# Performance work log

Hardware: AMD Instinct MI355X
Metric: run time of the kernel (lower is better)

Reference implementation:

```python
import jax, jax.numpy as jnp
import numpy as np

B, L, D, H, DK, DV = 2, 2048, 1024, 16, 64, 64
NEG_INF = -100000000.0


def setup_inputs() -> dict:
    key = jax.random.key(0)
    ks = jax.random.split(key, 10)
    s = 0.02
    inp = {
        "q": jax.random.normal(ks[0], (B, L, D), jnp.float32),
        "k": jax.random.normal(ks[1], (B, L, D), jnp.float32),
        "v": jax.random.normal(ks[2], (B, L, D), jnp.float32),
        "Wq": jax.random.normal(ks[3], (D, H * DK), jnp.float32) * s,
        "bq": jnp.zeros((H * DK,), jnp.float32),
        "Wk": jax.random.normal(ks[4], (D, H * DK), jnp.float32) * s,
        "bk": jnp.zeros((H * DK,), jnp.float32),
        "Wv": jax.random.normal(ks[5], (D, H * DV), jnp.float32) * s,
        "bv": jnp.zeros((H * DV,), jnp.float32),
        "W0": jax.random.normal(ks[6], (H * DV, D), jnp.float32) * s,
        "b0": jnp.zeros((D,), jnp.float32),
        "key_padding_mask": jax.random.uniform(ks[7], (B, L)) < 0.1,
        # 3D causal mask (B, Lq, Lk); True = masked
        "attn_mask": jnp.broadcast_to(jnp.triu(jnp.ones((L, L), bool), k=1), (B, L, L)),
    }
    return inp


def reference(q, k, v, Wq, bq, Wk, bk, Wv, bv, W0, b0, key_padding_mask, attn_mask):
    b, lq, _ = q.shape
    lk = k.shape[1]
    dk = Wq.shape[1] // H
    dv = Wv.shape[1] // H
    qh = (q @ Wq + bq).reshape(b, lq, H, dk)  # (B,Lq,H,dk)
    kh = (k @ Wk + bk).reshape(b, lk, H, dk)
    vh = (v @ Wv + bv).reshape(b, lk, H, dv)
    # scaled scores (B,H,Lq,Lk)
    attn = jnp.einsum("bqhd,bkhd->bhqk", qh, kh) / jnp.sqrt(jnp.float32(dk))
    # attn_mask (B,Lq,Lk): masked_fill semantics
    attn = jnp.where(attn_mask[:, None, :, :], NEG_INF, attn)
    # key_padding_mask (B,Lq): masks full query rows (broadcast over keys)
    attn = jnp.where(key_padding_mask[:, None, :, None], NEG_INF, attn)
    attn = jax.nn.softmax(attn, axis=-1)
    out = jnp.einsum("bhqk,bkhd->bqhd", attn, vh).reshape(b, lq, H * dv)
    out = out @ W0 + b0  # (B,Lq,D)
    return out, attn
```

## Files before the change

### kernel.cpp

```cpp
#include <hip/hip_runtime.h>

#define B_ 2
#define L_ 2048
#define D_ 1024
#define H_ 16
#define DKV 64
#define NEG_INF -1e8f

typedef float f32x4 __attribute__((ext_vector_type(4)));
typedef __bf16 bf16x8 __attribute__((ext_vector_type(8)));
typedef unsigned int u32x4 __attribute__((ext_vector_type(4)));
typedef unsigned int u32x2 __attribute__((ext_vector_type(2)));
typedef unsigned short u16x4 __attribute__((ext_vector_type(4)));

__device__ __forceinline__ unsigned short f2bfbits(float f) {
  unsigned int u = __builtin_bit_cast(unsigned int, f);
  unsigned int r = (u + 0x7FFFu + ((u >> 16) & 1u)) >> 16;
  return (unsigned short)r;
}
__device__ __forceinline__ __bf16 f2bf(float f) {
  return __builtin_bit_cast(__bf16, f2bfbits(f));
}
__device__ __forceinline__ float bf2f(unsigned short b) {
  unsigned int u = ((unsigned int)b) << 16;
  return __builtin_bit_cast(float, u);
}

__global__ __launch_bounds__(256) void norm_kpm_k(const void* __restrict__ raw,
                                                  unsigned char* __restrict__ kpmn) {
  __shared__ int flag;
  const int tid = threadIdx.x;
  if (tid == 0) flag = 0;
  __syncthreads();
  const unsigned* w = (const unsigned*)raw;
  unsigned bad = 0;
  for (int i = tid; i < 1024; i += 256) bad |= (w[i] > 1u) ? 1u : 0u;
  if (bad) flag = 1;
  __syncthreads();
  const bool u8 = (flag != 0);
  const unsigned char* u = (const unsigned char*)raw;
  for (int i = tid; i < B_ * L_; i += 256)
    kpmn[i] = u8 ? (u[i] != 0) : (w[i] != 0);
}

__global__ __launch_bounds__(256) void convert_x_k(
    const float* __restrict__ xq, const float* __restrict__ xk, const float* __restrict__ xv,
    unsigned short* __restrict__ oq, unsigned short* __restrict__ ok, unsigned short* __restrict__ ov)
{
  const int proj = blockIdx.y;
  const float* X = proj == 0 ? xq : (proj == 1 ? xk : xv);
  unsigned short* O = proj == 0 ? oq : (proj == 1 ? ok : ov);
  const long i8 = ((long)blockIdx.x * 256 + threadIdx.x) * 8;
  f32x4 a = *(const f32x4*)(X + i8);
  f32x4 b = *(const f32x4*)(X + i8 + 4);
  u32x4 p;
  p[0] = (unsigned)f2bfbits(a[0]) | ((unsigned)f2bfbits(a[1]) << 16);
  p[1] = (unsigned)f2bfbits(a[2]) | ((unsigned)f2bfbits(a[3]) << 16);
  p[2] = (unsigned)f2bfbits(b[0]) | ((unsigned)f2bfbits(b[1]) << 16);
  p[3] = (unsigned)f2bfbits(b[2]) | ((unsigned)f2bfbits(b[3]) << 16);
  *(u32x4*)(O + i8) = p;
}

__global__ __launch_bounds__(256) void convert_wt_k(
    const float* __restrict__ Wq, const float* __restrict__ Wk,
    const float* __restrict__ Wv, const float* __restrict__ W0,
    unsigned short* __restrict__ Wtq, unsigned short* __restrict__ Wtk,
    unsigned short* __restrict__ Wtv, unsigned short* __restrict__ W0t)
{
  __shared__ float Tl[64][65];
  const int m = blockIdx.z;
  const float* W = m == 0 ? Wq : (m == 1 ? Wk : (m == 2 ? Wv : W0));
  unsigned short* Wt = m == 0 ? Wtq : (m == 1 ? Wtk : (m == 2 ? Wtv : W0t));
  const int k0 = blockIdx.x * 64, n0 = blockIdx.y * 64;
  const int tid = threadIdx.x;
  #pragma unroll
  for (int it = 0; it < 4; ++it) {
    int idx = it * 256 + tid;
    int r = idx >> 4, c4 = (idx & 15) << 2;
    f32x4 x = *(const f32x4*)(W + (long)(k0 + r) * 1024 + n0 + c4);
    Tl[r][c4] = x[0]; Tl[r][c4 + 1] = x[1]; Tl[r][c4 + 2] = x[2]; Tl[r][c4 + 3] = x[3];
  }
  __syncthreads();
  #pragma unroll
  for (int it = 0; it < 2; ++it) {
    int idx = it * 256 + tid;
    int n = idx >> 3, c8 = (idx & 7) << 3;
    u32x4 p;
    #pragma unroll
    for (int j = 0; j < 4; ++j)
      p[j] = (unsigned)f2bfbits(Tl[c8 + 2 * j][n]) | ((unsigned)f2bfbits(Tl[c8 + 2 * j + 1][n]) << 16);
    *(u32x4*)(Wt + (long)(n0 + n) * 1024 + k0 + c8) = p;
  }
}

__global__ __launch_bounds__(256) void colsum_part_k(const unsigned short* __restrict__ vh,
                                                     float* __restrict__ part) {
  __shared__ float red[4][64];
  const int bid = blockIdx.x, tid = threadIdx.x;
  const int z = bid >> 3, seg = bid & 7;
  const int col = tid & 63, rgrp = tid >> 6;
  const long zoff = (long)z * L_ * DKV;
  float s = 0.f;
  #pragma unroll 4
  for (int i = 0; i < 64; ++i) {
    int r = seg * 256 + rgrp + 4 * i;
    s += bf2f(vh[zoff + (long)r * DKV + col]);
  }
  red[rgrp][col] = s;
  __syncthreads();
  if (tid < 64)
    part[(long)bid * 64 + tid] = red[0][tid] + red[1][tid] + red[2][tid] + red[3][tid];
}

__global__ __launch_bounds__(64) void colsum_final_k(const float* __restrict__ part,
                                                     float* __restrict__ colsumV) {
  const int z = blockIdx.x, col = threadIdx.x;
  float s = 0.f;
  #pragma unroll
  for (int seg = 0; seg < 8; ++seg) s += part[((long)z * 8 + seg) * 64 + col];
  colsumV[z * DKV + col] = s;
}

__global__ __launch_bounds__(256) void qkv_gemm_k(
    const unsigned short* __restrict__ xqb, const unsigned short* __restrict__ xkb,
    const unsigned short* __restrict__ xvb,
    const unsigned short* __restrict__ Wtq, const unsigned short* __restrict__ Wtk,
    const unsigned short* __restrict__ Wtv,
    const float* __restrict__ bq, const float* __restrict__ bk, const float* __restrict__ bv,
    unsigned short* __restrict__ oq, unsigned short* __restrict__ ok, unsigned short* __restrict__ ov)
{
  __shared__ __align__(16) unsigned short Al[128][72];
  __shared__ __align__(16) unsigned short Bl[128][72];
  const int proj = blockIdx.y;
  const unsigned short* X  = proj == 0 ? xqb : (proj == 1 ? xkb : xvb);
  const unsigned short* Wt = proj == 0 ? Wtq : (proj == 1 ? Wtk : Wtv);
  const float* bias = proj == 0 ? bq : (proj == 1 ? bk : bv);
  unsigned short* O = proj == 0 ? oq : (proj == 1 ? ok : ov);
  const int mt = blockIdx.x, zp = blockIdx.z;
  const int bb = zp >> 3, hp = zp & 7;
  const int tid = threadIdx.x, lane = tid & 63, w = tid >> 6, g = lane >> 4, l16 = lane & 15;
  const int wm = w >> 1, wn = w & 1;
  const long arow0 = (long)bb * L_ + mt * 128;
  const long brow0 = (long)hp * 128;

  const f32x4 zero4 = {0.f, 0.f, 0.f, 0.f};
  f32x4 acc[4][4];
  #pragma unroll
  for (int i = 0; i < 4; ++i)
    #pragma unroll
    for (int j = 0; j < 4; ++j) acc[i][j] = zero4;

  for (int kt = 0; kt < D_; kt += 64) {
    #pragma unroll
    for (int it = 0; it < 4; ++it) {
      int idx = it * 256 + tid;
      int r = idx >> 3, c8 = (idx & 7) << 3;
      *(u32x4*)&Al[r][c8] = *(const u32x4*)(X + (arow0 + r) * D_ + kt + c8);
      *(u32x4*)&Bl[r][c8] = *(const u32x4*)(Wt + (brow0 + r) * D_ + kt + c8);
    }
    __syncthreads();
    #pragma unroll
    for (int ks = 0; ks < 2; ++ks) {
      bf16x8 a[4], bv8[4];
      #pragma unroll
      for (int fm = 0; fm < 4; ++fm)
        a[fm] = *(const bf16x8*)&Al[wm * 64 + fm * 16 + l16][ks * 32 + g * 8];
      #pragma unroll
      for (int fn = 0; fn < 4; ++fn)
        bv8[fn] = *(const bf16x8*)&Bl[wn * 64 + fn * 16 + l16][ks * 32 + g * 8];
      #pragma unroll
      for (int fm = 0; fm < 4; ++fm)
        #pragma unroll
        for (int fn = 0; fn < 4; ++fn)
          acc[fm][fn] = __builtin_amdgcn_mfma_f32_16x16x32_bf16(a[fm], bv8[fn], acc[fm][fn], 0, 0, 0);
    }
    __syncthreads();
  }
  #pragma unroll
  for (int fm = 0; fm < 4; ++fm)
    #pragma unroll
    for (int fn = 0; fn < 4; ++fn)
      #pragma unroll
      for (int r = 0; r < 4; ++r) {
        int row = mt * 128 + wm * 64 + fm * 16 + g * 4 + r;
        int col = wn * 64 + fn * 16 + l16;
        float val = acc[fm][fn][r] + bias[hp * 128 + col];
        int zh = bb * H_ + hp * 2 + (col >> 6);
        O[(long)zh * L_ * 64 + (long)row * 64 + (col & 63)] = f2bfbits(val);
      }
}

__global__ __launch_bounds__(256) void oproj_gemm_k(
    const unsigned short* __restrict__ Ab, const unsigned short* __restrict__ W0t,
    const float* __restrict__ b0, float* __restrict__ out)
{
  __shared__ __align__(16) unsigned short Al[64][72];
  __shared__ __align__(16) unsigned short Bl[128][72];
  const int mt = blockIdx.x, nt = blockIdx.y;
  const int tid = threadIdx.x, lane = tid & 63, w = tid >> 6, g = lane >> 4, l16 = lane & 15;
  const int wm = w >> 1, wn = w & 1;

  const f32x4 zero4 = {0.f, 0.f, 0.f, 0.f};
  f32x4 acc[2][4];
  #pragma unroll
  for (int i = 0; i < 2; ++i)
    #pragma unroll
    for (int j = 0; j < 4; ++j) acc[i][j] = zero4;

  for (int kt = 0; kt < D_; kt += 64) {
    #pragma unroll
    for (int it = 0; it < 2; ++it) {
      int idx = it * 256 + tid;
      int r = idx >> 3, c8 = (idx & 7) << 3;
      *(u32x4*)&Al[r][c8] = *(const u32x4*)(Ab + (long)(mt * 64 + r) * D_ + kt + c8);
    }
    #pragma unroll
    for (int it = 0; it < 4; ++it) {
      int idx = it * 256 + tid;
      int r = idx >> 3, c8 = (idx & 7) << 3;
      *(u32x4*)&Bl[r][c8] = *(const u32x4*)(W0t + (long)(nt * 128 + r) * D_ + kt + c8);
    }
    __syncthreads();
    #pragma unroll
    for (int ks = 0; ks < 2; ++ks) {
      bf16x8 a[2], bv8[4];
      #pragma unroll
      for (int fm = 0; fm < 2; ++fm)
        a[fm] = *(const bf16x8*)&Al[wm * 32 + fm * 16 + l16][ks * 32 + g * 8];
      #pragma unroll
      for (int fn = 0; fn < 4; ++fn)
        bv8[fn] = *(const bf16x8*)&Bl[wn * 64 + fn * 16 + l16][ks * 32 + g * 8];
      #pragma unroll
      for (int fm = 0; fm < 2; ++fm)
        #pragma unroll
        for (int fn = 0; fn < 4; ++fn)
          acc[fm][fn] = __builtin_amdgcn_mfma_f32_16x16x32_bf16(a[fm], bv8[fn], acc[fm][fn], 0, 0, 0);
    }
    __syncthreads();
  }
  #pragma unroll
  for (int fm = 0; fm < 2; ++fm)
    #pragma unroll
    for (int fn = 0; fn < 4; ++fn)
      #pragma unroll
      for (int r = 0; r < 4; ++r) {
        int row = mt * 64 + wm * 32 + fm * 16 + g * 4 + r;
        int col = nt * 128 + wn * 64 + fn * 16 + l16;
        out[(long)row * D_ + col] = acc[fm][fn][r] + b0[col];
      }
}

__global__ __launch_bounds__(256) void attn_pv_k(
    const unsigned short* __restrict__ qh, const unsigned short* __restrict__ kh,
    const unsigned short* __restrict__ vh, const unsigned char* __restrict__ kpm,
    const float* __restrict__ colsumV, float* __restrict__ attn,
    unsigned short* __restrict__ oh)
{
  __shared__ __align__(16) char smem[64 * 68 * 4];
  auto Ql = (unsigned short (*)[72])smem;
  auto Pl = (float (*)[68])smem;
  __shared__ __align__(16) unsigned short Kl[64][72];
  __shared__ __align__(16) unsigned short Vl[64][72];
  __shared__ unsigned char padl[64];

  const int tid = threadIdx.x, lane = tid & 63, w = tid >> 6, g = lane >> 4, l16 = lane & 15;
  const int bid = blockIdx.x;
  const int z = bid & 31;
  const int sx = bid >> 5;
  const int q0 = sx * 64;
  const int b = z >> 4, h = z & 15;
  const long zoff = (long)z * L_ * DKV;
  const int rowbase = q0 + w * 16 + g * 4;

  #pragma unroll
  for (int it = 0; it < 2; ++it) {
    int f = it * 256 + tid;
    int r = f >> 3, c8 = (f & 7) << 3;
    *(u32x4*)&Ql[r][c8] = *(const u32x4*)(qh + zoff + (long)(q0 + r) * 64 + c8);
  }
  if (tid < 64) padl[tid] = kpm[b * L_ + q0 + tid];
  __syncthreads();
  bf16x8 a[2];
  #pragma unroll
  for (int ks = 0; ks < 2; ++ks)
    a[ks] = *(const bf16x8*)&Ql[w * 16 + l16][ks * 32 + g * 8];
  bool pad[4];
  #pragma unroll
  for (int r = 0; r < 4; ++r) pad[r] = padl[w * 16 + g * 4 + r] != 0;
  __syncthreads();

  float psum[4] = {0.f, 0.f, 0.f, 0.f};
  const f32x4 zero4 = {0.f, 0.f, 0.f, 0.f};
  f32x4 o[4];
  #pragma unroll
  for (int fn = 0; fn < 4; ++fn) o[fn] = zero4;

  for (int kt = 0; kt <= sx; ++kt) {
    #pragma unroll
    for (int it = 0; it < 2; ++it) {
      int f = it * 256 + tid;
      int r = f >> 3, c8 = (f & 7) << 3;
      *(u32x4*)&Kl[r][c8] = *(const u32x4*)(kh + zoff + (long)(kt * 64 + r) * 64 + c8);
    }
    #pragma unroll
    for (int it = 0; it < 4; ++it) {
      int f = it * 256 + tid;
      int kk = f >> 4, n4 = (f & 15) << 2;
      u16x4 u = *(const u16x4*)(vh + zoff + (long)(kt * 64 + kk) * 64 + n4);
      int sw = kk ^ (((n4 >> 2) & 7) << 3);
      Vl[n4 + 0][sw] = u[0]; Vl[n4 + 1][sw] = u[1];
      Vl[n4 + 2][sw] = u[2]; Vl[n4 + 3][sw] = u[3];
    }
    __syncthreads();
    f32x4 s[4];
    #pragma unroll
    for (int fn = 0; fn < 4; ++fn) {
      bf16x8 bv0 = *(const bf16x8*)&Kl[fn * 16 + l16][g * 8];
      bf16x8 bv1 = *(const bf16x8*)&Kl[fn * 16 + l16][32 + g * 8];
      f32x4 t = zero4;
      t = __builtin_amdgcn_mfma_f32_16x16x32_bf16(a[0], bv0, t, 0, 0, 0);
      t = __builtin_amdgcn_mfma_f32_16x16x32_bf16(a[1], bv1, t, 0, 0, 0);
      s[fn] = t;
    }
    #pragma unroll
    for (int fn = 0; fn < 4; ++fn)
      #pragma unroll
      for (int r = 0; r < 4; ++r) {
        int kk = kt * 64 + fn * 16 + l16;
        float sv = s[fn][r] * 0.125f;
        if (kk > rowbase + r) sv = NEG_INF;
        float p = __expf(sv - 12.0f);
        psum[r] += p;
        Pl[w * 16 + g * 4 + r][fn * 16 + l16] = p;
      }
    bf16x8 pa[2];
    #pragma unroll
    for (int ks = 0; ks < 2; ++ks) {
      f32x4 lo = *(const f32x4*)&Pl[w * 16 + l16][ks * 32 + g * 8];
      f32x4 hi = *(const f32x4*)&Pl[w * 16 + l16][ks * 32 + g * 8 + 4];
      bf16x8 t;
      #pragma unroll
      for (int i = 0; i < 4; ++i) { t[i] = f2bf(lo[i]); t[i + 4] = f2bf(hi[i]); }
      pa[ks] = t;
    }
    #pragma unroll
    for (int fn = 0; fn < 4; ++fn) {
      int dv = fn * 16 + l16;
      int swz = ((dv >> 2) & 7) << 3;
      bf16x8 vb0 = *(const bf16x8*)&Vl[dv][(0 * 32 + g * 8) ^ swz];
      bf16x8 vb1 = *(const bf16x8*)&Vl[dv][(1 * 32 + g * 8) ^ swz];
      o[fn] = __builtin_amdgcn_mfma_f32_16x16x32_bf16(pa[0], vb0, o[fn], 0, 0, 0);
      o[fn] = __builtin_amdgcn_mfma_f32_16x16x32_bf16(pa[1], vb1, o[fn], 0, 0, 0);
    }
    __syncthreads();
  }

  float linv[4];
  #pragma unroll
  for (int r = 0; r < 4; ++r) {
    float s = psum[r];
    #pragma unroll
    for (int d = 1; d < 16; d <<= 1) s += __shfl_xor(s, d);
    linv[r] = 1.f / s;
  }
  const float invL = 1.0f / (float)L_;

  float* arow = attn + ((long)z * L_ + q0 + w * 16) * L_;
  for (int kt = 0; kt <= sx; ++kt) {
    #pragma unroll
    for (int it = 0; it < 2; ++it) {
      int f = it * 256 + tid;
      int r = f >> 3, c8 = (f & 7) << 3;
      *(u32x4*)&Kl[r][c8] = *(const u32x4*)(kh + zoff + (long)(kt * 64 + r) * 64 + c8);
    }
    __syncthreads();
    f32x4 s[4];
    #pragma unroll
    for (int fn = 0; fn < 4; ++fn) {
      bf16x8 bv0 = *(const bf16x8*)&Kl[fn * 16 + l16][g * 8];
      bf16x8 bv1 = *(const bf16x8*)&Kl[fn * 16 + l16][32 + g * 8];
      f32x4 t = zero4;
      t = __builtin_amdgcn_mfma_f32_16x16x32_bf16(a[0], bv0, t, 0, 0, 0);
      t = __builtin_amdgcn_mfma_f32_16x16x32_bf16(a[1], bv1, t, 0, 0, 0);
      s[fn] = t;
    }
    #pragma unroll
    for (int fn = 0; fn < 4; ++fn)
      #pragma unroll
      for (int r = 0; r < 4; ++r) {
        int kk = kt * 64 + fn * 16 + l16;
        float sv = s[fn][r] * 0.125f;
        if (kk > rowbase + r) sv = NEG_INF;
        float p = pad[r] ? invL : __expf(sv - 12.0f) * linv[r];
        __builtin_nontemporal_store(p, &arow[(long)(g * 4 + r) * L_ + kt * 64 + fn * 16 + l16]);
      }
    __syncthreads();
  }
  for (int kt = sx + 1; kt < L_ / 64; ++kt) {
    #pragma unroll
    for (int it = 0; it < 4; ++it) {
      int f = it * 256 + tid;
      int r = f >> 4, c4 = (f & 15) << 2;
      float vvv = padl[r] ? invL : 0.f;
      f32x4 ov = {vvv, vvv, vvv, vvv};
      __builtin_nontemporal_store(ov, (f32x4*)&attn[((long)z * L_ + q0 + r) * L_ + kt * 64 + c4]);
    }
  }

  #pragma unroll
  for (int fn = 0; fn < 4; ++fn)
    #pragma unroll
    for (int r = 0; r < 4; ++r) {
      int qq = rowbase + r;
      int dv = fn * 16 + l16;
      float val = pad[r] ? invL * colsumV[z * DKV + dv] : o[fn][r] * linv[r];
      oh[((long)b * L_ + qq) * (H_ * DKV) + h * DKV + dv] = f2bfbits(val);
    }
}

extern "C" void kernel_launch(void* const* d_in, const int* in_sizes, int n_in,
                              void* d_out, int out_size, void* d_ws, size_t ws_size,
                              hipStream_t stream) {
  (void)in_sizes; (void)n_in; (void)out_size; (void)ws_size;
  const float* q  = (const float*)d_in[0];
  const float* k  = (const float*)d_in[1];
  const float* v  = (const float*)d_in[2];
  const float* Wq = (const float*)d_in[3];
  const float* bq = (const float*)d_in[4];
  const float* Wk = (const float*)d_in[5];
  const float* bk = (const float*)d_in[6];
  const float* Wv = (const float*)d_in[7];
  const float* bv = (const float*)d_in[8];
  const float* W0 = (const float*)d_in[9];
  const float* b0 = (const float*)d_in[10];
  const void*  kpm_raw = d_in[11];

  float* out  = (float*)d_out;
  float* attn = out + (long)B_ * L_ * D_;

  const long XE = (long)B_ * L_ * D_;
  const long HEAD_ELEMS = (long)B_ * H_ * L_ * DKV;
  unsigned short* qh  = (unsigned short*)d_ws;
  unsigned short* kh  = qh + HEAD_ELEMS;
  unsigned short* vh  = kh + HEAD_ELEMS;
  unsigned short* xqb = vh + HEAD_ELEMS;
  unsigned short* xkb = xqb + XE;
  unsigned short* xvb = xkb + XE;
  unsigned short* oh  = xqb;
  unsigned short* Wtq = xvb + XE;
  unsigned short* Wtk = Wtq + (long)D_ * D_;
  unsigned short* Wtv = Wtk + (long)D_ * D_;
  unsigned short* W0t = Wtv + (long)D_ * D_;
  float* colsumV = (float*)(W0t + (long)D_ * D_);
  float* part    = colsumV + 32 * 64;
  unsigned char* kpmn = (unsigned char*)(part + 256 * 64);

  dim3 blk(256);

  norm_kpm_k<<<1, blk, 0, stream>>>(kpm_raw, kpmn);
  convert_x_k<<<dim3(XE / (256 * 8), 3), blk, 0, stream>>>(q, k, v, xqb, xkb, xvb);
  convert_wt_k<<<dim3(16, 16, 4), blk, 0, stream>>>(Wq, Wk, Wv, W0, Wtq, Wtk, Wtv, W0t);

  qkv_gemm_k<<<dim3(L_ / 128, 3, B_ * (H_ / 2)), blk, 0, stream>>>(
      xqb, xkb, xvb, Wtq, Wtk, Wtv, bq, bk, bv, qh, kh, vh);

  colsum_part_k<<<dim3(256), blk, 0, stream>>>(vh, part);
  colsum_final_k<<<dim3(32), dim3(64), 0, stream>>>(part, colsumV);

  attn_pv_k<<<dim3(1024), blk, 0, stream>>>(
      qh, kh, vh, kpmn, colsumV, attn, oh);

  oproj_gemm_k<<<dim3(B_ * L_ / 64, D_ / 128), blk, 0, stream>>>(
      oh, W0t, b0, out);
}
```

Baseline: 259.8 us.

## Merge prep kernels and register-prefetch K/V tiles in attention kernel

Three preprocessing kernels (mask normalisation, activation conversion, weight transpose) become one launch dispatched by block index, saving launch overhead. The attention kernel now prefetches the next K/V tile into registers while the current tile is computed. Its second pass handles two K tiles per barrier by reusing the V shared buffer, which halves the syncs. A launch-bounds occupancy hint of 4 is added, which may limit registers and risk spills.

```diff
diff --git a/kernel.cpp b/kernel.cpp
--- a/kernel.cpp
+++ b/kernel.cpp
@@ -26,70 +26,68 @@
   return __builtin_bit_cast(float, u);
 }
 
-__global__ __launch_bounds__(256) void norm_kpm_k(const void* __restrict__ raw,
-                                                  unsigned char* __restrict__ kpmn) {
-  __shared__ int flag;
-  const int tid = threadIdx.x;
-  if (tid == 0) flag = 0;
-  __syncthreads();
-  const unsigned* w = (const unsigned*)raw;
-  unsigned bad = 0;
-  for (int i = tid; i < 1024; i += 256) bad |= (w[i] > 1u) ? 1u : 0u;
-  if (bad) flag = 1;
-  __syncthreads();
-  const bool u8 = (flag != 0);
-  const unsigned char* u = (const unsigned char*)raw;
-  for (int i = tid; i < B_ * L_; i += 256)
-    kpmn[i] = u8 ? (u[i] != 0) : (w[i] != 0);
-}
-
-__global__ __launch_bounds__(256) void convert_x_k(
+__global__ __launch_bounds__(256) void prep_k(
     const float* __restrict__ xq, const float* __restrict__ xk, const float* __restrict__ xv,
-    unsigned short* __restrict__ oq, unsigned short* __restrict__ ok, unsigned short* __restrict__ ov)
-{
-  const int proj = blockIdx.y;
-  const float* X = proj == 0 ? xq : (proj == 1 ? xk : xv);
-  unsigned short* O = proj == 0 ? oq : (proj == 1 ? ok : ov);
-  const long i8 = ((long)blockIdx.x * 256 + threadIdx.x) * 8;
-  f32x4 a = *(const f32x4*)(X + i8);
-  f32x4 b = *(const f32x4*)(X + i8 + 4);
-  u32x4 p;
-  p[0] = (unsigned)f2bfbits(a[0]) | ((unsigned)f2bfbits(a[1]) << 16);
-  p[1] = (unsigned)f2bfbits(a[2]) | ((unsigned)f2bfbits(a[3]) << 16);
-  p[2] = (unsigned)f2bfbits(b[0]) | ((unsigned)f2bfbits(b[1]) << 16);
-  p[3] = (unsigned)f2bfbits(b[2]) | ((unsigned)f2bfbits(b[3]) << 16);
-  *(u32x4*)(O + i8) = p;
-}
-
-__global__ __launch_bounds__(256) void convert_wt_k(
     const float* __restrict__ Wq, const float* __restrict__ Wk,
     const float* __restrict__ Wv, const float* __restrict__ W0,
+    const void* __restrict__ kpm_raw,
+    unsigned short* __restrict__ oq, unsigned short* __restrict__ ok, unsigned short* __restrict__ ov,
     unsigned short* __restrict__ Wtq, unsigned short* __restrict__ Wtk,
-    unsigned short* __restrict__ Wtv, unsigned short* __restrict__ W0t)
+    unsigned short* __restrict__ Wtv, unsigned short* __restrict__ W0t,
+    unsigned char* __restrict__ kpmn)
 {
   __shared__ float Tl[64][65];
-  const int m = blockIdx.z;
-  const float* W = m == 0 ? Wq : (m == 1 ? Wk : (m == 2 ? Wv : W0));
-  unsigned short* Wt = m == 0 ? Wtq : (m == 1 ? Wtk : (m == 2 ? Wtv : W0t));
-  const int k0 = blockIdx.x * 64, n0 = blockIdx.y * 64;
-  const int tid = threadIdx.x;
-  #pragma unroll
-  for (int it = 0; it < 4; ++it) {
-    int idx = it * 256 + tid;
-    int r = idx >> 4, c4 = (idx & 15) << 2;
-    f32x4 x = *(const f32x4*)(W + (long)(k0 + r) * 1024 + n0 + c4);
-    Tl[r][c4] = x[0]; Tl[r][c4 + 1] = x[1]; Tl[r][c4 + 2] = x[2]; Tl[r][c4 + 3] = x[3];
-  }
-  __syncthreads();
-  #pragma unroll
-  for (int it = 0; it < 2; ++it) {
-    int idx = it * 256 + tid;
-    int n = idx >> 3, c8 = (idx & 7) << 3;
+  const int bid = blockIdx.x, tid = threadIdx.x;
+  if (bid < 6144) {
+    const int proj = bid >> 11;
+    const float* X = proj == 0 ? xq : (proj == 1 ? xk : xv);
+    unsigned short* O = proj == 0 ? oq : (proj == 1 ? ok : ov);
+    const long i8 = ((long)(bid & 2047) * 256 + tid) * 8;
+    f32x4 a = *(const f32x4*)(X + i8);
+    f32x4 b = *(const f32x4*)(X + i8 + 4);
     u32x4 p;
-    #pragma unroll
-    for (int j = 0; j < 4; ++j)
-      p[j] = (unsigned)f2bfbits(Tl[c8 + 2 * j][n]) | ((unsigned)f2bfbits(Tl[c8 + 2 * j + 1][n]) << 16);
-    *(u32x4*)(Wt + (long)(n0 + n) * 1024 + k0 + c8) = p;
+    p[0] = (unsigned)f2bfbits(a[0]) | ((unsigned)f2bfbits(a[1]) << 16);
+    p[1] = (unsigned)f2bfbits(a[2]) | ((unsigned)f2bfbits(a[3]) << 16);
+    p[2] = (unsigned)f2bfbits(b[0]) | ((unsigned)f2bfbits(b[1]) << 16);
+    p[3] = (unsigned)f2bfbits(b[2]) | ((unsigned)f2bfbits(b[3]) << 16);
+    *(u32x4*)(O + i8) = p;
+  } else if (bid < 7168) {
+    const int wid = bid - 6144;
+    const int m = wid >> 8, t = wid & 255;
+    const float* W = m == 0 ? Wq : (m == 1 ? Wk : (m == 2 ? Wv : W0));
+    unsigned short* Wt = m == 0 ? Wtq : (m == 1 ? Wtk : (m == 2 ? Wtv : W0t));
+    const int k0 = ((t >> 4) & 15) * 64, n0 = (t & 15) * 64;
+    #pragma unroll
+    for (int it = 0; it < 4; ++it) {
+      int idx = it * 256 + tid;
+      int r = idx >> 4, c4 = (idx & 15) << 2;
+      f32x4 x = *(const f32x4*)(W + (long)(k0 + r) * 1024 + n0 + c4);
+      Tl[r][c4] = x[0]; Tl[r][c4 + 1] = x[1]; Tl[r][c4 + 2] = x[2]; Tl[r][c4 + 3] = x[3];
+    }
+    __syncthreads();
+    #pragma unroll
+    for (int it = 0; it < 2; ++it) {
+      int idx = it * 256 + tid;
+      int n = idx >> 3, c8 = (idx & 7) << 3;
+      u32x4 p;
+      #pragma unroll
+      for (int j = 0; j < 4; ++j)
+        p[j] = (unsigned)f2bfbits(Tl[c8 + 2 * j][n]) | ((unsigned)f2bfbits(Tl[c8 + 2 * j + 1][n]) << 16);
+      *(u32x4*)(Wt + (long)(n0 + n) * 1024 + k0 + c8) = p;
+    }
+  } else {
+    __shared__ int flag;
+    if (tid == 0) flag = 0;
+    __syncthreads();
+    const unsigned* w = (const unsigned*)kpm_raw;
+    unsigned bad = 0;
+    for (int i = tid; i < 1024; i += 256) bad |= (w[i] > 1u) ? 1u : 0u;
+    if (bad) flag = 1;
+    __syncthreads();
+    const bool u8 = (flag != 0);
+    const unsigned char* u = (const unsigned char*)kpm_raw;
+    for (int i = tid; i < B_ * L_; i += 256)
+      kpmn[i] = u8 ? (u[i] != 0) : (w[i] != 0);
   }
 }
 
@@ -250,7 +248,7 @@
       }
 }
 
-__global__ __launch_bounds__(256) void attn_pv_k(
+__global__ __launch_bounds__(256, 4) void attn_pv_k(
     const unsigned short* __restrict__ qh, const unsigned short* __restrict__ kh,
     const unsigned short* __restrict__ vh, const unsigned char* __restrict__ kpm,
     const float* __restrict__ colsumV, float* __restrict__ attn,
@@ -272,6 +270,9 @@
   const long zoff = (long)z * L_ * DKV;
   const int rowbase = q0 + w * 16 + g * 4;
 
+  const int kr = tid >> 3, kc8 = (tid & 7) << 3;
+  const int vk = tid >> 4, vn4 = (tid & 15) << 2;
+
   #pragma unroll
   for (int it = 0; it < 2; ++it) {
     int f = it * 256 + tid;
@@ -295,23 +296,36 @@
   #pragma unroll
   for (int fn = 0; fn < 4; ++fn) o[fn] = zero4;
 
+  u32x4 Kreg[2];
+  u16x4 Vreg[4];
+  #pragma unroll
+  for (int it = 0; it < 2; ++it)
+    Kreg[it] = *(const u32x4*)(kh + zoff + (long)(kr + it * 32) * 64 + kc8);
+  #pragma unroll
+  for (int it = 0; it < 4; ++it)
+    Vreg[it] = *(const u16x4*)(vh + zoff + (long)(vk + it * 16) * 64 + vn4);
+
   for (int kt = 0; kt <= sx; ++kt) {
     #pragma unroll
-    for (int it = 0; it < 2; ++it) {
-      int f = it * 256 + tid;
-      int r = f >> 3, c8 = (f & 7) << 3;
-      *(u32x4*)&Kl[r][c8] = *(const u32x4*)(kh + zoff + (long)(kt * 64 + r) * 64 + c8);
-    }
+    for (int it = 0; it < 2; ++it)
+      *(u32x4*)&Kl[kr + it * 32][kc8] = Kreg[it];
     #pragma unroll
     for (int it = 0; it < 4; ++it) {
-      int f = it * 256 + tid;
-      int kk = f >> 4, n4 = (f & 15) << 2;
-      u16x4 u = *(const u16x4*)(vh + zoff + (long)(kt * 64 + kk) * 64 + n4);
-      int sw = kk ^ (((n4 >> 2) & 7) << 3);
-      Vl[n4 + 0][sw] = u[0]; Vl[n4 + 1][sw] = u[1];
-      Vl[n4 + 2][sw] = u[2]; Vl[n4 + 3][sw] = u[3];
-    }
-    __syncthreads();
+      int kk = vk + it * 16;
+      int sw = kk ^ (((vn4 >> 2) & 7) << 3);
+      Vl[vn4 + 0][sw] = Vreg[it][0]; Vl[vn4 + 1][sw] = Vreg[it][1];
+      Vl[vn4 + 2][sw] = Vreg[it][2]; Vl[vn4 + 3][sw] = Vreg[it][3];
+    }
+    __syncthreads();
+    if (kt < sx) {
+      const long noff = zoff + (long)((kt + 1) * 64) * 64;
+      #pragma unroll
+      for (int it = 0; it < 2; ++it)
+        Kreg[it] = *(const u32x4*)(kh + noff + (long)(kr + it * 32) * 64 + kc8);
+      #pragma unroll
+      for (int it = 0; it < 4; ++it)
+        Vreg[it] = *(const u16x4*)(vh + noff + (long)(vk + it * 16) * 64 + vn4);
+    }
     f32x4 s[4];
     #pragma unroll
     for (int fn = 0; fn < 4; ++fn) {
@@ -366,15 +380,35 @@
   const float invL = 1.0f / (float)L_;
 
   float* arow = attn + ((long)z * L_ + q0 + w * 16) * L_;
-  for (int kt = 0; kt <= sx; ++kt) {
-    #pragma unroll
-    for (int it = 0; it < 2; ++it) {
-      int f = it * 256 + tid;
-      int r = f >> 3, c8 = (f & 7) << 3;
-      *(u32x4*)&Kl[r][c8] = *(const u32x4*)(kh + zoff + (long)(kt * 64 + r) * 64 + c8);
-    }
-    __syncthreads();
-    f32x4 s[4];
+  u32x4 K2reg[2];
+  #pragma unroll
+  for (int it = 0; it < 2; ++it)
+    Kreg[it] = *(const u32x4*)(kh + zoff + (long)(kr + it * 32) * 64 + kc8);
+  if (1 <= sx)
+    #pragma unroll
+    for (int it = 0; it < 2; ++it)
+      K2reg[it] = *(const u32x4*)(kh + zoff + (long)(64 + kr + it * 32) * 64 + kc8);
+
+  for (int kt = 0; kt <= sx; kt += 2) {
+    const bool has2 = (kt + 1 <= sx);
+    #pragma unroll
+    for (int it = 0; it < 2; ++it)
+      *(u32x4*)&Kl[kr + it * 32][kc8] = Kreg[it];
+    if (has2)
+      #pragma unroll
+      for (int it = 0; it < 2; ++it)
+        *(u32x4*)&Vl[kr + it * 32][kc8] = K2reg[it];
+    __syncthreads();
+    if (kt + 2 <= sx) {
+      const long noff = zoff + (long)((kt + 2) * 64) * 64;
+      #pragma unroll
+      for (int it = 0; it < 2; ++it)
+        Kreg[it] = *(const u32x4*)(kh + noff + (long)(kr + it * 32) * 64 + kc8);
+      if (kt + 3 <= sx)
+        #pragma unroll
+        for (int it = 0; it < 2; ++it)
+          K2reg[it] = *(const u32x4*)(kh + noff + (long)(64 + kr + it * 32) * 64 + kc8);
+    }
     #pragma unroll
     for (int fn = 0; fn < 4; ++fn) {
       bf16x8 bv0 = *(const bf16x8*)&Kl[fn * 16 + l16][g * 8];
@@ -382,18 +416,33 @@
       f32x4 t = zero4;
       t = __builtin_amdgcn_mfma_f32_16x16x32_bf16(a[0], bv0, t, 0, 0, 0);
       t = __builtin_amdgcn_mfma_f32_16x16x32_bf16(a[1], bv1, t, 0, 0, 0);
-      s[fn] = t;
-    }
-    #pragma unroll
-    for (int fn = 0; fn < 4; ++fn)
       #pragma unroll
       for (int r = 0; r < 4; ++r) {
         int kk = kt * 64 + fn * 16 + l16;
-        float sv = s[fn][r] * 0.125f;
+        float sv = t[r] * 0.125f;
         if (kk > rowbase + r) sv = NEG_INF;
         float p = pad[r] ? invL : __expf(sv - 12.0f) * linv[r];
-        __builtin_nontemporal_store(p, &arow[(long)(g * 4 + r) * L_ + kt * 64 + fn * 16 + l16]);
+        __builtin_nontemporal_store(p, &arow[(long)(g * 4 + r) * L_ + kk]);
       }
+    }
+    if (has2) {
+      #pragma unroll
+      for (int fn = 0; fn < 4; ++fn) {
+        bf16x8 bv0 = *(const bf16x8*)&Vl[fn * 16 + l16][g * 8];
+        bf16x8 bv1 = *(const bf16x8*)&Vl[fn * 16 + l16][32 + g * 8];
+        f32x4 t = zero4;
+        t = __builtin_amdgcn_mfma_f32_16x16x32_bf16(a[0], bv0, t, 0, 0, 0);
+        t = __builtin_amdgcn_mfma_f32_16x16x32_bf16(a[1], bv1, t, 0, 0, 0);
+        #pragma unroll
+        for (int r = 0; r < 4; ++r) {
+          int kk = (kt + 1) * 64 + fn * 16 + l16;
+          float sv = t[r] * 0.125f;
+          if (kk > rowbase + r) sv = NEG_INF;
+          float p = pad[r] ? invL : __expf(sv - 12.0f) * linv[r];
+          __builtin_nontemporal_store(p, &arow[(long)(g * 4 + r) * L_ + kk]);
+        }
+      }
+    }
     __syncthreads();
   }
   for (int kt = sx + 1; kt < L_ / 64; ++kt) {
@@ -457,9 +506,9 @@
 
   dim3 blk(256);
 
-  norm_kpm_k<<<1, blk, 0, stream>>>(kpm_raw, kpmn);
-  convert_x_k<<<dim3(XE / (256 * 8), 3), blk, 0, stream>>>(q, k, v, xqb, xkb, xvb);
-  convert_wt_k<<<dim3(16, 16, 4), blk, 0, stream>>>(Wq, Wk, Wv, W0, Wtq, Wtk, Wtv, W0t);
+  prep_k<<<dim3(7169), blk, 0, stream>>>(
+      q, k, v, Wq, Wk, Wv, W0, kpm_raw,
+      xqb, xkb, xvb, Wtq, Wtk, Wtv, W0t, kpmn);
 
   qkv_gemm_k<<<dim3(L_ / 128, 3, B_ * (H_ / 2)), blk, 0, stream>>>(
       xqb, xkb, xvb, Wtq, Wtk, Wtv, bq, bk, bv, qh, kh, vh);
```

Result: no change. 258.7 us (-0.4%).
